# Kernel optimization log

Hardware: AMD Instinct MI355X
Metric: run time of the kernel (lower is better)

## Reference

```python
import jax, jax.numpy as jnp
import numpy as np

B, R, O, D = 32, 3136, 20, 32  # batch, rays(=56*56), objects, d_object
H = W = 56


def setup_inputs() -> dict:
    key = jax.random.key(0)
    k1, k2, k3 = jax.random.split(key, 3)
    form_decoding = jax.random.normal(k1, (B, R, O, D), dtype=jnp.float32)
    depth = jax.random.normal(k2, (B, R, O), dtype=jnp.float32)
    # original: transmitance = -t**2 (non-positive) so exp(transmitance) <= 1
    transmitance = -jax.random.uniform(k3, (B, R, O), dtype=jnp.float32)
    return {"form_decoding": form_decoding, "depth": depth, "transmitance": transmitance}


def reference(form_decoding, depth, transmitance):
    # NeRF-style alpha compositing over objects along each ray.
    o = depth.shape[-1]
    # pairwise depth comparison: sigmoid(1000*(D[...,o] - D[...,O])), zero diag
    diff = depth[..., :, None] - depth[..., None, :]              # [b,r,o,O]
    comp = jax.nn.sigmoid(1000.0 * diff) * (1.0 - jnp.eye(o, dtype=depth.dtype))
    # accumulated log-transmittance of objects in front
    acc = jnp.einsum('brO,broO->bro', transmitance, comp)         # [b,r,o]
    ponderation = jnp.exp(acc) * (1.0 - jnp.exp(transmitance))    # [b,r,o]
    result = jnp.einsum('bro,brod->brd', ponderation, form_decoding)  # [b,r,d]
    b = form_decoding.shape[0]
    result = result.reshape(b, H, W, -1).transpose(0, 3, 1, 2)    # [b,d,H,W]
    return (result, ponderation)
```

## Files before the change

kernel.cpp:

```cpp
#include <hip/hip_runtime.h>

#define NB 32
#define NR 3136
#define NO 20
#define ND 32
#define RPB 16
#define BLOCK (RPB * 32)

__global__ __launch_bounds__(BLOCK) void ray_composite(
    const float* __restrict__ form,
    const float* __restrict__ depth,
    const float* __restrict__ trans,
    float* __restrict__ out_res,
    float* __restrict__ out_pond)
{
  __shared__ float res_lds[RPB][36];
  __shared__ float pond_lds[RPB * NO];

  const int t    = threadIdx.x;
  const int rib  = t >> 5;
  const int lane = t & 31;
  const int ray0 = blockIdx.x * RPB;
  const int ray  = ray0 + rib;
  const int b    = ray0 / NR;
  const int r0   = ray0 - b * NR;

  float d_o = 0.f, t_o = 0.f;
  if (lane < NO) {
    d_o = depth[(size_t)ray * NO + lane];
    t_o = trans[(size_t)ray * NO + lane];
  }
  float acc = 0.f;
#pragma unroll
  for (int j = 0; j < NO; ++j) {
    const float dj = __shfl(d_o, j, 32);
    const float tj = __shfl(t_o, j, 32);
    const float s  = 1.f / (1.f + __expf(-1000.f * (d_o - dj)));
    if (j != lane) acc += tj * s;
  }
  float pond = __expf(acc) * (1.f - __expf(t_o));
  if (lane >= NO) pond = 0.f;
  if (lane < NO) pond_lds[rib * NO + lane] = pond;

  const int c  = lane & 7;
  const int og = lane >> 3;
  const float* fbase = form + (size_t)ray * (NO * ND);
  float4 accv = make_float4(0.f, 0.f, 0.f, 0.f);
#pragma unroll
  for (int k = 0; k < 5; ++k) {
    const int o = og + 4 * k;
    const float p = __shfl(pond, o, 32);
    const float4 v = *reinterpret_cast<const float4*>(fbase + o * ND + c * 4);
    accv.x += p * v.x; accv.y += p * v.y; accv.z += p * v.z; accv.w += p * v.w;
  }
#pragma unroll
  for (int m = 8; m <= 16; m <<= 1) {
    accv.x += __shfl_xor(accv.x, m, 32);
    accv.y += __shfl_xor(accv.y, m, 32);
    accv.z += __shfl_xor(accv.z, m, 32);
    accv.w += __shfl_xor(accv.w, m, 32);
  }
  if (lane < 8)
    *reinterpret_cast<float4*>(&res_lds[rib][lane * 4]) = accv;

  __syncthreads();

  {
    const int d  = t >> 4;
    const int rr = t & 15;
    out_res[(size_t)b * (ND * NR) + (size_t)d * NR + r0 + rr] = res_lds[rr][d];
  }
  if (t < RPB * NO)
    out_pond[(size_t)ray0 * NO + t] = pond_lds[t];
}

extern "C" void kernel_launch(void* const* d_in, const int* in_sizes, int n_in,
                              void* d_out, int out_size, void* d_ws, size_t ws_size,
                              hipStream_t stream) {
  const float* form  = (const float*)d_in[0];
  const float* depth = (const float*)d_in[1];
  const float* trans = (const float*)d_in[2];

  float* out_res  = (float*)d_out;
  float* out_pond = out_res + (size_t)NB * ND * NR;

  dim3 grid((NB * NR) / RPB);
  dim3 block(BLOCK);
  ray_composite<<<grid, block, 0, stream>>>(form, depth, trans, out_res, out_pond);
}
```

Measured before the change: 50.08 us.

## Process two rays per warp with vectorized staging and wider stores

Doubles rays per block to 32 while keeping 512 threads, so each 32-lane group handles two rays, giving more independent loads in flight per thread. Depth and transmittance are staged into LDS through coalesced float4 loads, and the result and ponderation stores become float2 writes. This is meant to cut per-element load/store instructions and improve memory-level parallelism, at the cost of more registers per thread and an extra barrier.

```diff
diff --git a/kernel.cpp b/kernel.cpp
--- a/kernel.cpp
+++ b/kernel.cpp
@@ -4,8 +4,8 @@
 #define NR 3136
 #define NO 20
 #define ND 32
-#define RPB 16
-#define BLOCK (RPB * 32)
+#define RPB 32
+#define BLOCK 512
 
 __global__ __launch_bounds__(BLOCK) void ray_composite(
     const float* __restrict__ form,
@@ -14,6 +14,7 @@
     float* __restrict__ out_res,
     float* __restrict__ out_pond)
 {
+  __shared__ float stage[2 * RPB * NO];
   __shared__ float res_lds[RPB][36];
   __shared__ float pond_lds[RPB * NO];
 
@@ -21,57 +22,82 @@
   const int rib  = t >> 5;
   const int lane = t & 31;
   const int ray0 = blockIdx.x * RPB;
-  const int ray  = ray0 + rib;
   const int b    = ray0 / NR;
   const int r0   = ray0 - b * NR;
 
-  float d_o = 0.f, t_o = 0.f;
+  if (t < 160)
+    reinterpret_cast<float4*>(stage)[t] =
+        reinterpret_cast<const float4*>(depth + (size_t)ray0 * NO)[t];
+  else if (t < 320)
+    reinterpret_cast<float4*>(stage + RPB * NO)[t - 160] =
+        reinterpret_cast<const float4*>(trans + (size_t)ray0 * NO)[t - 160];
+  __syncthreads();
+
+  float dA = 0.f, tA = 0.f, dB = 0.f, tB = 0.f;
   if (lane < NO) {
-    d_o = depth[(size_t)ray * NO + lane];
-    t_o = trans[(size_t)ray * NO + lane];
+    dA = stage[rib * NO + lane];
+    tA = stage[RPB * NO + rib * NO + lane];
+    dB = stage[(rib + 16) * NO + lane];
+    tB = stage[RPB * NO + (rib + 16) * NO + lane];
   }
-  float acc = 0.f;
+  float accA = 0.f, accB = 0.f;
 #pragma unroll
   for (int j = 0; j < NO; ++j) {
-    const float dj = __shfl(d_o, j, 32);
-    const float tj = __shfl(t_o, j, 32);
-    const float s  = 1.f / (1.f + __expf(-1000.f * (d_o - dj)));
-    if (j != lane) acc += tj * s;
+    const float djA = __shfl(dA, j, 32), tjA = __shfl(tA, j, 32);
+    const float djB = __shfl(dB, j, 32), tjB = __shfl(tB, j, 32);
+    if (j != lane) {
+      accA += tjA / (1.f + __expf(-1000.f * (dA - djA)));
+      accB += tjB / (1.f + __expf(-1000.f * (dB - djB)));
+    }
   }
-  float pond = __expf(acc) * (1.f - __expf(t_o));
-  if (lane >= NO) pond = 0.f;
-  if (lane < NO) pond_lds[rib * NO + lane] = pond;
+  float pondA = __expf(accA) * (1.f - __expf(tA));
+  float pondB = __expf(accB) * (1.f - __expf(tB));
+  if (lane >= NO) { pondA = 0.f; pondB = 0.f; }
+  if (lane < NO) {
+    pond_lds[rib * NO + lane]        = pondA;
+    pond_lds[(rib + 16) * NO + lane] = pondB;
+  }
 
   const int c  = lane & 7;
   const int og = lane >> 3;
-  const float* fbase = form + (size_t)ray * (NO * ND);
-  float4 accv = make_float4(0.f, 0.f, 0.f, 0.f);
+  const float* fA = form + (size_t)(ray0 + rib) * (NO * ND);
+  const float* fB = form + (size_t)(ray0 + rib + 16) * (NO * ND);
+  float4 aA = make_float4(0.f, 0.f, 0.f, 0.f);
+  float4 aB = make_float4(0.f, 0.f, 0.f, 0.f);
 #pragma unroll
   for (int k = 0; k < 5; ++k) {
     const int o = og + 4 * k;
-    const float p = __shfl(pond, o, 32);
-    const float4 v = *reinterpret_cast<const float4*>(fbase + o * ND + c * 4);
-    accv.x += p * v.x; accv.y += p * v.y; accv.z += p * v.z; accv.w += p * v.w;
+    const float pA = __shfl(pondA, o, 32);
+    const float pB = __shfl(pondB, o, 32);
+    const float4 vA = *reinterpret_cast<const float4*>(fA + o * ND + c * 4);
+    const float4 vB = *reinterpret_cast<const float4*>(fB + o * ND + c * 4);
+    aA.x += pA * vA.x; aA.y += pA * vA.y; aA.z += pA * vA.z; aA.w += pA * vA.w;
+    aB.x += pB * vB.x; aB.y += pB * vB.y; aB.z += pB * vB.z; aB.w += pB * vB.w;
   }
 #pragma unroll
   for (int m = 8; m <= 16; m <<= 1) {
-    accv.x += __shfl_xor(accv.x, m, 32);
-    accv.y += __shfl_xor(accv.y, m, 32);
-    accv.z += __shfl_xor(accv.z, m, 32);
-    accv.w += __shfl_xor(accv.w, m, 32);
+    aA.x += __shfl_xor(aA.x, m, 32); aA.y += __shfl_xor(aA.y, m, 32);
+    aA.z += __shfl_xor(aA.z, m, 32); aA.w += __shfl_xor(aA.w, m, 32);
+    aB.x += __shfl_xor(aB.x, m, 32); aB.y += __shfl_xor(aB.y, m, 32);
+    aB.z += __shfl_xor(aB.z, m, 32); aB.w += __shfl_xor(aB.w, m, 32);
   }
-  if (lane < 8)
-    *reinterpret_cast<float4*>(&res_lds[rib][lane * 4]) = accv;
-
+  if (lane < 8) {
+    *reinterpret_cast<float4*>(&res_lds[rib][lane * 4])      = aA;
+    *reinterpret_cast<float4*>(&res_lds[rib + 16][lane * 4]) = aB;
+  }
   __syncthreads();
 
   {
-    const int d  = t >> 4;
-    const int rr = t & 15;
-    out_res[(size_t)b * (ND * NR) + (size_t)d * NR + r0 + rr] = res_lds[rr][d];
+    const int d = t >> 4;
+    const int j = t & 15;
+    float2 v = make_float2(res_lds[2 * j][d], res_lds[2 * j + 1][d]);
+    *reinterpret_cast<float2*>(out_res + (size_t)b * (ND * NR) +
+                               (size_t)d * NR + r0 + 2 * j) = v;
   }
-  if (t < RPB * NO)
-    out_pond[(size_t)ray0 * NO + t] = pond_lds[t];
+  if (t < RPB * NO / 2) {
+    float2 v = make_float2(pond_lds[2 * t], pond_lds[2 * t + 1]);
+    *reinterpret_cast<float2*>(out_pond + (size_t)ray0 * NO + 2 * t) = v;
+  }
 }
 
 extern "C" void kernel_launch(void* const* d_in, const int* in_sizes, int n_in,
```

Result: slower. 51.86 us (+3.5%).
